# Kernel tuning notes

Measured on AMD Instinct MI355X. Metric: run time of the kernel, lower is better.

## Reference

```python
import jax, jax.numpy as jnp
import numpy as np

DIM = 1024
DIM_HEAD = 64
HEADS = DIM // DIM_HEAD
SCALE = DIM_HEAD ** -0.5


def setup_inputs() -> dict:
    key = jax.random.key(0)
    k1, k2, k3, k4 = jax.random.split(key, 4)
    x = jax.random.normal(k1, (2, 2048, DIM), dtype=jnp.float32)
    W_qkv = jax.random.normal(k2, (DIM, 3 * DIM), dtype=jnp.float32) * (DIM ** -0.5)
    W_out = jax.random.normal(k3, (DIM, DIM), dtype=jnp.float32) * (DIM ** -0.5)
    b_out = jax.random.normal(k4, (DIM,), dtype=jnp.float32) * 0.01
    return {"x": x, "W_qkv": W_qkv, "W_out": W_out, "b_out": b_out}


def reference(x, W_qkv, W_out, b_out):
    b, n, _ = x.shape
    qkv = x @ W_qkv  # [b, n, 3*dim]
    q, k, v = jnp.split(qkv, 3, axis=-1)
    # b n (h d) -> b h n d
    def split_heads(t):
        return t.reshape(b, n, HEADS, DIM_HEAD).transpose(0, 2, 1, 3)
    q, k, v = map(split_heads, (q, k, v))
    sim = jnp.einsum('bhid,bhjd->bhij', q, k) * SCALE  # full O(n^2) scores
    attn = jax.nn.softmax(sim, axis=-1)
    res = jnp.einsum('bhij,bhjd->bhid', attn, v)
    res = res.transpose(0, 2, 1, 3).reshape(b, n, DIM)  # b h n d -> b n (h d)
    return res @ W_out + b_out
```

## Files before the change

### kernel.cpp

```cpp
#include <hip/hip_runtime.h>

#define DIMM 1024
#define HEADS 16
#define DH 64
#define NSEQ 2048
#define BATCH 2
#define MTOT (BATCH*NSEQ)
#define NQKV (3*DIMM)
#define QSCALE 0.1803368801111243f

typedef unsigned short u16;
typedef __bf16 bf16x8 __attribute__((ext_vector_type(8)));
typedef __bf16 bf16x4 __attribute__((ext_vector_type(4)));
typedef float f32x4 __attribute__((ext_vector_type(4)));
typedef u16 u16x8 __attribute__((ext_vector_type(8)));
typedef u16 u16x4 __attribute__((ext_vector_type(4)));

typedef const __attribute__((address_space(1))) void* gp1_t;
typedef __attribute__((address_space(3))) void* lp3_t;

static __device__ __forceinline__ u16 cvt1(float f){
  return __builtin_bit_cast(u16, (__bf16)f);
}

__global__ __launch_bounds__(256) void conv_bf16_kernel(const float* __restrict__ in,
                                                        u16* __restrict__ out, int n){
  int i = (blockIdx.x * 256 + threadIdx.x) * 8;
  if (i >= n) return;
  float4 a = *(const float4*)(in + i);
  float4 b = *(const float4*)(in + i + 4);
  u16x8 o;
  o[0] = cvt1(a.x); o[1] = cvt1(a.y); o[2] = cvt1(a.z); o[3] = cvt1(a.w);
  o[4] = cvt1(b.x); o[5] = cvt1(b.y); o[6] = cvt1(b.z); o[7] = cvt1(b.w);
  *(u16x8*)(out + i) = o;
}

__global__ __launch_bounds__(256) void transpose_bf16_kernel(const float* __restrict__ in,
                                                             u16* __restrict__ out, int K, int N){
  __shared__ float tile[32][33];
  int n0 = blockIdx.x * 32, k0 = blockIdx.y * 32;
  int tx = threadIdx.x, ty = threadIdx.y;
  #pragma unroll
  for (int r = 0; r < 32; r += 8)
    tile[ty + r][tx] = in[(size_t)(k0 + ty + r) * N + n0 + tx];
  __syncthreads();
  #pragma unroll
  for (int r = 0; r < 32; r += 8)
    out[(size_t)(n0 + ty + r) * K + k0 + tx] = cvt1(tile[tx][ty + r]);
}

__global__ __launch_bounds__(256) void gemm_qkv_kernel(const u16* __restrict__ A, const u16* __restrict__ Bt,
                                                       u16* __restrict__ qb, u16* __restrict__ kb,
                                                       u16* __restrict__ vTb){
  __shared__ __align__(16) u16 As[128 * 32];
  __shared__ __align__(16) u16 Bs[128 * 32];
  const int tid = threadIdx.x;
  const int wave = tid >> 6, lane = tid & 63;
  const int wm = wave >> 1, wn = wave & 1;
  const int l15 = lane & 15, lhi = lane >> 4;
  const int bcol = blockIdx.x, brow = blockIdx.y;
  const int K = DIMM;
  const u16* Ab = A + (size_t)brow * 128 * K;
  const u16* Bb = Bt + (size_t)bcol * 128 * K;
  f32x4 acc[4][4] = {};
  for (int kt = 0; kt < K; kt += 32){
    #pragma unroll
    for (int i = 0; i < 2; i++){
      int chunk = i * 256 + tid;
      int row = chunk >> 2, kc = chunk & 3;
      __builtin_amdgcn_global_load_lds((gp1_t)(Ab + (size_t)row * K + kt + kc * 8),
                                       (lp3_t)(As + (i * 256 + wave * 64) * 8), 16, 0, 0);
      __builtin_amdgcn_global_load_lds((gp1_t)(Bb + (size_t)row * K + kt + kc * 8),
                                       (lp3_t)(Bs + (i * 256 + wave * 64) * 8), 16, 0, 0);
    }
    __syncthreads();
    bf16x8 af[4], bfr[4];
    #pragma unroll
    for (int mt = 0; mt < 4; mt++)
      af[mt] = *(const bf16x8*)(As + (wm * 64 + mt * 16 + l15) * 32 + lhi * 8);
    #pragma unroll
    for (int nt = 0; nt < 4; nt++)
      bfr[nt] = *(const bf16x8*)(Bs + (wn * 64 + nt * 16 + l15) * 32 + lhi * 8);
    #pragma unroll
    for (int mt = 0; mt < 4; mt++)
      #pragma unroll
      for (int nt = 0; nt < 4; nt++)
        acc[mt][nt] = __builtin_amdgcn_mfma_f32_16x16x32_bf16(af[mt], bfr[nt], acc[mt][nt], 0, 0, 0);
    __syncthreads();
  }
  const int ncolbase = bcol * 128 + wn * 64;
  const int mrowbase = brow * 128 + wm * 64;
  #pragma unroll
  for (int mt = 0; mt < 4; mt++){
    #pragma unroll
    for (int nt = 0; nt < 4; nt++){
      int n = ncolbase + nt * 16 + l15;
      int which = n >> 10, c = n & 1023;
      int h = c >> 6, d = c & 63;
      int m0 = mrowbase + mt * 16 + lhi * 4;
      int b = m0 >> 11, row = m0 & 2047;
      if (which == 0){
        #pragma unroll
        for (int r = 0; r < 4; r++)
          qb[(((size_t)(b * HEADS + h)) * NSEQ + row + r) * DH + d] = cvt1(acc[mt][nt][r] * QSCALE);
      } else if (which == 1){
        #pragma unroll
        for (int r = 0; r < 4; r++)
          kb[(((size_t)(b * HEADS + h)) * NSEQ + row + r) * DH + d] = cvt1(acc[mt][nt][r]);
      } else {
        u16x4 pv;
        #pragma unroll
        for (int r = 0; r < 4; r++) pv[r] = cvt1(acc[mt][nt][r]);
        *(u16x4*)(vTb + (((size_t)(b * HEADS + h)) * DH + d) * NSEQ + row) = pv;
      }
    }
  }
}

__global__ __launch_bounds__(256) void attn_kernel(const u16* __restrict__ qg, const u16* __restrict__ kg,
                                                   const u16* __restrict__ vTg, u16* __restrict__ resb){
  __shared__ __align__(16) u16 Ks[64 * 72];
  __shared__ __align__(16) u16 VTs[64 * 72];
  __shared__ __align__(16) u16 Ps[4][16 * 72];
  const int tid = threadIdx.x;
  const int wave = tid >> 6, lane = tid & 63;
  const int l15 = lane & 15, lhi = lane >> 4;
  const int qt = blockIdx.x, bh = blockIdx.y;
  const u16* Qb = qg + ((size_t)bh * NSEQ + qt * 64 + wave * 16) * DH;
  const u16* Kb = kg + (size_t)bh * NSEQ * DH;
  const u16* Vb = vTg + (size_t)bh * DH * NSEQ;
  bf16x8 qa[2];
  #pragma unroll
  for (int c = 0; c < 2; c++)
    qa[c] = *(const bf16x8*)(Qb + l15 * DH + c * 32 + lhi * 8);
  f32x4 oacc[4] = {};
  float lrun = 0.f;

  const int srow = tid >> 3, sch = tid & 7;

  {
    float4 k0 = *(const float4*)(Kb + (size_t)srow * DH + sch * 8);
    float4 k1 = *(const float4*)(Kb + (size_t)(srow + 32) * DH + sch * 8);
    float4 v0 = *(const float4*)(Vb + (size_t)srow * NSEQ + sch * 8);
    float4 v1 = *(const float4*)(Vb + (size_t)(srow + 32) * NSEQ + sch * 8);
    *(float4*)(Ks + srow * 72 + sch * 8) = k0;
    *(float4*)(Ks + (srow + 32) * 72 + sch * 8) = k1;
    *(float4*)(VTs + srow * 72 + sch * 8) = v0;
    *(float4*)(VTs + (srow + 32) * 72 + sch * 8) = v1;
  }
  __syncthreads();

  for (int kt = 0; kt < NSEQ / 64; kt++){
    const bool more = (kt + 1 < NSEQ / 64);
    float4 nk0, nk1, nv0, nv1;
    if (more){
      const u16* kn = Kb + (size_t)(kt + 1) * 64 * DH;
      const u16* vn = Vb + (size_t)(kt + 1) * 64;
      nk0 = *(const float4*)(kn + (size_t)srow * DH + sch * 8);
      nk1 = *(const float4*)(kn + (size_t)(srow + 32) * DH + sch * 8);
      nv0 = *(const float4*)(vn + (size_t)srow * NSEQ + sch * 8);
      nv1 = *(const float4*)(vn + (size_t)(srow + 32) * NSEQ + sch * 8);
    }
    f32x4 st[4];
    #pragma unroll
    for (int nt = 0; nt < 4; nt++){
      f32x4 z = {};
      #pragma unroll
      for (int c = 0; c < 2; c++){
        bf16x8 kf = *(const bf16x8*)(Ks + (nt * 16 + l15) * 72 + c * 32 + lhi * 8);
        z = __builtin_amdgcn_mfma_f32_16x16x32_bf16(kf, qa[c], z, 0, 0, 0);
      }
      st[nt] = z;
    }
    float rsum = 0.f;
    #pragma unroll
    for (int nt = 0; nt < 4; nt++){
      float p0 = exp2f(st[nt][0]), p1 = exp2f(st[nt][1]);
      float p2 = exp2f(st[nt][2]), p3 = exp2f(st[nt][3]);
      rsum += (p0 + p1) + (p2 + p3);
      bf16x4 pw; pw[0] = (__bf16)p0; pw[1] = (__bf16)p1; pw[2] = (__bf16)p2; pw[3] = (__bf16)p3;
      *(bf16x4*)(&Ps[wave][l15 * 72 + nt * 16 + lhi * 4]) = pw;
    }
    lrun += rsum;
    #pragma unroll
    for (int c = 0; c < 2; c++){
      bf16x8 pf = *(const bf16x8*)(&Ps[wave][l15 * 72 + c * 32 + lhi * 8]);
      #pragma unroll
      for (int dt = 0; dt < 4; dt++){
        bf16x8 vf = *(const bf16x8*)(VTs + (dt * 16 + l15) * 72 + c * 32 + lhi * 8);
        oacc[dt] = __builtin_amdgcn_mfma_f32_16x16x32_bf16(pf, vf, oacc[dt], 0, 0, 0);
      }
    }
    __syncthreads();
    if (more){
      *(float4*)(Ks + srow * 72 + sch * 8) = nk0;
      *(float4*)(Ks + (srow + 32) * 72 + sch * 8) = nk1;
      *(float4*)(VTs + srow * 72 + sch * 8) = nv0;
      *(float4*)(VTs + (srow + 32) * 72 + sch * 8) = nv1;
    }
    __syncthreads();
  }
  lrun += __shfl_xor(lrun, 16);
  lrun += __shfl_xor(lrun, 32);
  const int b = bh >> 4, h = bh & 15;
  #pragma unroll
  for (int r = 0; r < 4; r++){
    float lr = __shfl(lrun, (lane & 48) | (lhi * 4 + r));
    float inv = 1.0f / lr;
    int row = qt * 64 + wave * 16 + lhi * 4 + r;
    size_t base = ((size_t)b * NSEQ + row) * DIMM + h * DH;
    #pragma unroll
    for (int dt = 0; dt < 4; dt++)
      resb[base + dt * 16 + l15] = cvt1(oacc[dt][r] * inv);
  }
}

__global__ __launch_bounds__(256) void gemm_out_kernel(const u16* __restrict__ A, const u16* __restrict__ Bt,
                                                       const float* __restrict__ bias, float* __restrict__ out){
  __shared__ __align__(16) u16 As[128 * 32];
  __shared__ __align__(16) u16 Bs[128 * 32];
  const int tid = threadIdx.x;
  const int wave = tid >> 6, lane = tid & 63;
  const int wm = wave >> 1, wn = wave & 1;
  const int l15 = lane & 15, lhi = lane >> 4;
  const int bcol = blockIdx.x, brow = blockIdx.y;
  const int K = DIMM;
  const u16* Ab = A + (size_t)brow * 128 * K;
  const u16* Bb = Bt + (size_t)bcol * 128 * K;
  f32x4 acc[4][4] = {};
  for (int kt = 0; kt < K; kt += 32){
    #pragma unroll
    for (int i = 0; i < 2; i++){
      int chunk = i * 256 + tid;
      int row = chunk >> 2, kc = chunk & 3;
      __builtin_amdgcn_global_load_lds((gp1_t)(Ab + (size_t)row * K + kt + kc * 8),
                                       (lp3_t)(As + (i * 256 + wave * 64) * 8), 16, 0, 0);
      __builtin_amdgcn_global_load_lds((gp1_t)(Bb + (size_t)row * K + kt + kc * 8),
                                       (lp3_t)(Bs + (i * 256 + wave * 64) * 8), 16, 0, 0);
    }
    __syncthreads();
    bf16x8 af[4], bfr[4];
    #pragma unroll
    for (int mt = 0; mt < 4; mt++)
      af[mt] = *(const bf16x8*)(As + (wm * 64 + mt * 16 + l15) * 32 + lhi * 8);
    #pragma unroll
    for (int nt = 0; nt < 4; nt++)
      bfr[nt] = *(const bf16x8*)(Bs + (wn * 64 + nt * 16 + l15) * 32 + lhi * 8);
    #pragma unroll
    for (int mt = 0; mt < 4; mt++)
      #pragma unroll
      for (int nt = 0; nt < 4; nt++)
        acc[mt][nt] = __builtin_amdgcn_mfma_f32_16x16x32_bf16(af[mt], bfr[nt], acc[mt][nt], 0, 0, 0);
    __syncthreads();
  }
  const int ncolbase = bcol * 128 + wn * 64;
  const int mrowbase = brow * 128 + wm * 64;
  #pragma unroll
  for (int mt = 0; mt < 4; mt++){
    #pragma unroll
    for (int nt = 0; nt < 4; nt++){
      #pragma unroll
      for (int r = 0; r < 4; r++){
        int m = mrowbase + mt * 16 + lhi * 4 + r;
        int n = ncolbase + nt * 16 + l15;
        out[(size_t)m * DIMM + n] = acc[mt][nt][r] + bias[n];
      }
    }
  }
}

extern "C" void kernel_launch(void* const* d_in, const int* in_sizes, int n_in,
                              void* d_out, int out_size, void* d_ws, size_t ws_size,
                              hipStream_t stream){
  const float* x    = (const float*)d_in[0];
  const float* Wqkv = (const float*)d_in[1];
  const float* Wout = (const float*)d_in[2];
  const float* bout = (const float*)d_in[3];
  float* out = (float*)d_out;

  u16* xb    = (u16*)d_ws;
  u16* wqkvT = xb    + (size_t)MTOT * DIMM;
  u16* woutT = wqkvT + (size_t)NQKV * DIMM;
  u16* qb    = woutT + (size_t)DIMM * DIMM;
  u16* kb    = qb    + (size_t)BATCH * HEADS * NSEQ * DH;
  u16* vTb   = kb    + (size_t)BATCH * HEADS * NSEQ * DH;
  u16* resb  = xb;
  if (ws_size < (size_t)41943040) return;

  conv_bf16_kernel<<<(MTOT * DIMM) / 2048, 256, 0, stream>>>(x, xb, MTOT * DIMM);
  transpose_bf16_kernel<<<dim3(NQKV / 32, DIMM / 32), dim3(32, 8), 0, stream>>>(Wqkv, wqkvT, DIMM, NQKV);
  transpose_bf16_kernel<<<dim3(DIMM / 32, DIMM / 32), dim3(32, 8), 0, stream>>>(Wout, woutT, DIMM, DIMM);
  gemm_qkv_kernel<<<dim3(NQKV / 128, MTOT / 128), 256, 0, stream>>>(xb, wqkvT, qb, kb, vTb);
  attn_kernel<<<dim3(NSEQ / 64, BATCH * HEADS), 256, 0, stream>>>(qb, kb, vTb, resb);
  gemm_out_kernel<<<dim3(DIMM / 128, MTOT / 128), 256, 0, stream>>>(resb, woutT, bout, out);
}
```

Baseline: 213.9 us.

## Double attention query tile to 128 rows per block and merge prep kernels

The attention kernel now runs 512 threads (8 waves) per block, each block covering 128 query rows, so every staged K/V tile in LDS is reused by twice as many waves and each thread loads half as much per iteration. The grid is halved to 512 blocks. Separately, the x conversion and the two weight transposes are merged into one launch that dispatches on block index, removing two kernel launches. The risks are fewer blocks to spread across the CUs and more waves stalling at each barrier.

```diff
diff --git a/kernel.cpp b/kernel.cpp
--- a/kernel.cpp
+++ b/kernel.cpp
@@ -23,23 +23,27 @@
   return __builtin_bit_cast(u16, (__bf16)f);
 }
 
-__global__ __launch_bounds__(256) void conv_bf16_kernel(const float* __restrict__ in,
-                                                        u16* __restrict__ out, int n){
-  int i = (blockIdx.x * 256 + threadIdx.x) * 8;
-  if (i >= n) return;
-  float4 a = *(const float4*)(in + i);
-  float4 b = *(const float4*)(in + i + 4);
-  u16x8 o;
-  o[0] = cvt1(a.x); o[1] = cvt1(a.y); o[2] = cvt1(a.z); o[3] = cvt1(a.w);
-  o[4] = cvt1(b.x); o[5] = cvt1(b.y); o[6] = cvt1(b.z); o[7] = cvt1(b.w);
-  *(u16x8*)(out + i) = o;
-}
-
-__global__ __launch_bounds__(256) void transpose_bf16_kernel(const float* __restrict__ in,
-                                                             u16* __restrict__ out, int K, int N){
+__global__ __launch_bounds__(256) void prep_kernel(const float* __restrict__ x, u16* __restrict__ xb,
+                                                   const float* __restrict__ Wqkv, u16* __restrict__ wqkvT,
+                                                   const float* __restrict__ Wout, u16* __restrict__ woutT){
   __shared__ float tile[32][33];
-  int n0 = blockIdx.x * 32, k0 = blockIdx.y * 32;
-  int tx = threadIdx.x, ty = threadIdx.y;
+  const int id = blockIdx.x, tid = threadIdx.x;
+  if (id < 2048){
+    int i = (id * 256 + tid) * 8;
+    float4 a = *(const float4*)(x + i);
+    float4 b = *(const float4*)(x + i + 4);
+    u16x8 o;
+    o[0] = cvt1(a.x); o[1] = cvt1(a.y); o[2] = cvt1(a.z); o[3] = cvt1(a.w);
+    o[4] = cvt1(b.x); o[5] = cvt1(b.y); o[6] = cvt1(b.z); o[7] = cvt1(b.w);
+    *(u16x8*)(xb + i) = o;
+    return;
+  }
+  const float* in; u16* out; int N, bx, by;
+  if (id < 5120){ in = Wqkv; out = wqkvT; N = NQKV; bx = (id - 2048) % 96; by = (id - 2048) / 96; }
+  else          { in = Wout; out = woutT; N = DIMM; bx = (id - 5120) % 32; by = (id - 5120) / 32; }
+  const int K = DIMM;
+  int n0 = bx * 32, k0 = by * 32;
+  int tx = tid & 31, ty = tid >> 5;
   #pragma unroll
   for (int r = 0; r < 32; r += 8)
     tile[ty + r][tx] = in[(size_t)(k0 + ty + r) * N + n0 + tx];
@@ -117,16 +121,16 @@
   }
 }
 
-__global__ __launch_bounds__(256) void attn_kernel(const u16* __restrict__ qg, const u16* __restrict__ kg,
+__global__ __launch_bounds__(512) void attn_kernel(const u16* __restrict__ qg, const u16* __restrict__ kg,
                                                    const u16* __restrict__ vTg, u16* __restrict__ resb){
   __shared__ __align__(16) u16 Ks[64 * 72];
   __shared__ __align__(16) u16 VTs[64 * 72];
-  __shared__ __align__(16) u16 Ps[4][16 * 72];
+  __shared__ __align__(16) u16 Ps[8][16 * 72];
   const int tid = threadIdx.x;
   const int wave = tid >> 6, lane = tid & 63;
   const int l15 = lane & 15, lhi = lane >> 4;
   const int qt = blockIdx.x, bh = blockIdx.y;
-  const u16* Qb = qg + ((size_t)bh * NSEQ + qt * 64 + wave * 16) * DH;
+  const u16* Qb = qg + ((size_t)bh * NSEQ + qt * 128 + wave * 16) * DH;
   const u16* Kb = kg + (size_t)bh * NSEQ * DH;
   const u16* Vb = vTg + (size_t)bh * DH * NSEQ;
   bf16x8 qa[2];
@@ -140,26 +144,20 @@
 
   {
     float4 k0 = *(const float4*)(Kb + (size_t)srow * DH + sch * 8);
-    float4 k1 = *(const float4*)(Kb + (size_t)(srow + 32) * DH + sch * 8);
     float4 v0 = *(const float4*)(Vb + (size_t)srow * NSEQ + sch * 8);
-    float4 v1 = *(const float4*)(Vb + (size_t)(srow + 32) * NSEQ + sch * 8);
     *(float4*)(Ks + srow * 72 + sch * 8) = k0;
-    *(float4*)(Ks + (srow + 32) * 72 + sch * 8) = k1;
     *(float4*)(VTs + srow * 72 + sch * 8) = v0;
-    *(float4*)(VTs + (srow + 32) * 72 + sch * 8) = v1;
   }
   __syncthreads();
 
   for (int kt = 0; kt < NSEQ / 64; kt++){
     const bool more = (kt + 1 < NSEQ / 64);
-    float4 nk0, nk1, nv0, nv1;
+    float4 nk0, nv0;
     if (more){
       const u16* kn = Kb + (size_t)(kt + 1) * 64 * DH;
       const u16* vn = Vb + (size_t)(kt + 1) * 64;
       nk0 = *(const float4*)(kn + (size_t)srow * DH + sch * 8);
-      nk1 = *(const float4*)(kn + (size_t)(srow + 32) * DH + sch * 8);
       nv0 = *(const float4*)(vn + (size_t)srow * NSEQ + sch * 8);
-      nv1 = *(const float4*)(vn + (size_t)(srow + 32) * NSEQ + sch * 8);
     }
     f32x4 st[4];
     #pragma unroll
@@ -194,9 +192,7 @@
     __syncthreads();
     if (more){
       *(float4*)(Ks + srow * 72 + sch * 8) = nk0;
-      *(float4*)(Ks + (srow + 32) * 72 + sch * 8) = nk1;
       *(float4*)(VTs + srow * 72 + sch * 8) = nv0;
-      *(float4*)(VTs + (srow + 32) * 72 + sch * 8) = nv1;
     }
     __syncthreads();
   }
@@ -207,7 +203,7 @@
   for (int r = 0; r < 4; r++){
     float lr = __shfl(lrun, (lane & 48) | (lhi * 4 + r));
     float inv = 1.0f / lr;
-    int row = qt * 64 + wave * 16 + lhi * 4 + r;
+    int row = qt * 128 + wave * 16 + lhi * 4 + r;
     size_t base = ((size_t)b * NSEQ + row) * DIMM + h * DH;
     #pragma unroll
     for (int dt = 0; dt < 4; dt++)
@@ -287,10 +283,8 @@
   u16* resb  = xb;
   if (ws_size < (size_t)41943040) return;
 
-  conv_bf16_kernel<<<(MTOT * DIMM) / 2048, 256, 0, stream>>>(x, xb, MTOT * DIMM);
-  transpose_bf16_kernel<<<dim3(NQKV / 32, DIMM / 32), dim3(32, 8), 0, stream>>>(Wqkv, wqkvT, DIMM, NQKV);
-  transpose_bf16_kernel<<<dim3(DIMM / 32, DIMM / 32), dim3(32, 8), 0, stream>>>(Wout, woutT, DIMM, DIMM);
+  prep_kernel<<<2048 + 3072 + 1024, 256, 0, stream>>>(x, xb, Wqkv, wqkvT, Wout, woutT);
   gemm_qkv_kernel<<<dim3(NQKV / 128, MTOT / 128), 256, 0, stream>>>(xb, wqkvT, qb, kb, vTb);
-  attn_kernel<<<dim3(NSEQ / 64, BATCH * HEADS), 256, 0, stream>>>(qb, kb, vTb, resb);
+  attn_kernel<<<dim3(NSEQ / 128, BATCH * HEADS), 512, 0, stream>>>(qb, kb, vTb, resb);
   gemm_out_kernel<<<dim3(DIMM / 128, MTOT / 128), 256, 0, stream>>>(resb, woutT, bout, out);
 }
```

After: 197.7 us. 7.6% less time.
